# Optimization experiments

Hardware: AMD Instinct MI355X
Metric: run time of the kernel (lower is better)

## Reference

```python
import jax, jax.numpy as jnp
import numpy as np

B = 524288          # batch size
C = 64              # continuous dims
D = 8               # categorical dims
NCAT = 6            # categories per dim -> 6**8 = 1679616 total
NB = 21             # ceil(log2(6**8)) binary dims


def setup_inputs() -> dict:
    key = jax.random.key(0)
    k1, k2, k3 = jax.random.split(key, 3)
    inputs_continuous = jax.random.normal(k1, (B, C), dtype=jnp.float32)
    inputs_categorical = jax.random.randint(k2, (B, D), 0, NCAT, dtype=jnp.int32)
    # uniform dequantization noise in (0,1); keep away from 0 so log() is finite
    dequantization_noise = jax.random.uniform(k3, (B, 2 * NB), dtype=jnp.float32,
                                              minval=0.01, maxval=1.0)
    num_per_dim = jnp.full((D,), NCAT, dtype=jnp.int32)
    # category_factors[i] = prod(num_per_dim[:i]) (mixed-radix factors)
    category_factors = jnp.concatenate(
        [jnp.ones((1,), jnp.int32), jnp.cumprod(num_per_dim[:-1])]).astype(jnp.int32)
    binary_mask = (2 ** jnp.arange(NB - 1, -1, -1)).astype(jnp.int32)
    return {
        "inputs_continuous": inputs_continuous,
        "inputs_categorical": inputs_categorical,
        "dequantization_noise": dequantization_noise,
        "category_factors": category_factors,
        "binary_mask": binary_mask,
    }


def reference(inputs_continuous, inputs_categorical, dequantization_noise,
              category_factors, binary_mask):
    b = inputs_categorical.shape[0]
    nb = binary_mask.shape[0]
    # mixed-radix encode categories to a single decimal code: [B]
    decimal_encoded = jnp.sum(category_factors * inputs_categorical, axis=-1)
    # binary encode: [B, nb] bool
    binary_encoded = (decimal_encoded[:, None] & binary_mask) != 0
    # View noise as [B, nb, 2]; torch code gathers/scatters flat indices
    # 2i + (0 if bit else 1) for max slot, 2i + (1 if bit else 0) for min slot.
    view = dequantization_noise.reshape(b, nb, 2)
    v0, v1 = view[..., 0], view[..., 1]
    max_v = jnp.where(binary_encoded, v0, v1)
    min_v = jnp.where(binary_encoded, v1, v0)
    rescaling_log_probs = -jnp.sum(jnp.log(max_v), axis=-1)  # [B]
    new_min = min_v * max_v  # scatter-multiply into the min slots
    n0 = jnp.where(binary_encoded, max_v, new_min)
    n1 = jnp.where(binary_encoded, new_min, max_v)
    noise_out = jnp.stack([n0, n1], axis=-1).reshape(b, 2 * nb)
    out_continuous = jnp.concatenate([inputs_continuous, noise_out], axis=1)
    # uniform dequantizer: log prob of U(0,1) samples is 0
    dequantization_log_probs = jnp.zeros((b,), out_continuous.dtype)
    return out_continuous, dequantization_log_probs - rescaling_log_probs
```

## Files before the change

kernel.cpp:

```cpp
#include <hip/hip_runtime.h>


typedef float f4 __attribute__((ext_vector_type(4)));

constexpr int OUT_COLS = 106;
constexpr int OCTS_PER_WAVE = 2;
constexpr int WAVES = 4;
constexpr int ROWS_PER_BLOCK = WAVES * OCTS_PER_WAVE * 8;
constexpr int OUT_STAGE = 848;
constexpr int LG_STRIDE = 24;
constexpr int SLOT = OUT_STAGE + 8 * LG_STRIDE;

__global__ __launch_bounds__(256) void dequant_oct_kernel(
    const float* __restrict__ cont,
    const int*   __restrict__ cat,
    const float* __restrict__ noise,
    float* __restrict__ out,
    int B)
{
    __shared__ __align__(16) float sbuf[WAVES * OCTS_PER_WAVE * SLOT];

    const int tid  = threadIdx.x;
    const int wave = tid >> 6;
    const int lane = tid & 63;
    const int base = blockIdx.x * ROWS_PER_BLOCK + wave * (OCTS_PER_WAVE * 8);

#pragma unroll
    for (int qq = 0; qq < OCTS_PER_WAVE; ++qq) {
        const int r0 = base + 8 * qq;
        if (r0 < B) {
            float* buf = sbuf + (wave * OCTS_PER_WAVE + qq) * SLOT;
            float* lgb = buf + OUT_STAGE;

            const float* cp = cont + (size_t)r0 * 64;
            const f4 c0 = __builtin_nontemporal_load(
                reinterpret_cast<const f4*>(cp) + lane);
            const f4 c1 = __builtin_nontemporal_load(
                reinterpret_cast<const f4*>(cp) + 64 + lane);

            const float* np = noise + (size_t)r0 * 42;
            f4 n0 = __builtin_nontemporal_load(
                reinterpret_cast<const f4*>(np) + lane);
            f4 n1 = {1.f, 1.f, 1.f, 1.f};
            if (lane < 20)
                n1 = __builtin_nontemporal_load(
                    reinterpret_cast<const f4*>(np) + 64 + lane);

            int dec = 0;
            if (lane < 8) {
                const int4 a = *reinterpret_cast<const int4*>(cat + (size_t)(r0 + lane) * 8);
                const int4 b = *reinterpret_cast<const int4*>(cat + (size_t)(r0 + lane) * 8 + 4);
                dec = ((((((b.w * 6 + b.z) * 6 + b.y) * 6 + b.x) * 6
                         + a.w) * 6 + a.z) * 6 + a.y) * 6 + a.x;
            }

            auto do_pair = [&](int p, float va, float vb) {
                const int r = (p * 781) >> 14;
                const int j = p - 21 * r;
                const int dr  = __shfl(dec, r);
                const int bit = (dr >> (20 - j)) & 1;
                const float mx = bit ? va : vb;
                const float mn = bit ? vb : va;
                const float nm = mn * mx;
                float2 o;
                o.x = bit ? mx : nm;
                o.y = bit ? nm : mx;
                *reinterpret_cast<float2*>(buf + r * OUT_COLS + 64 + 2 * j) = o;
                lgb[r * LG_STRIDE + j] = __logf(mx);
            };
            do_pair(2 * lane,     n0.x, n0.y);
            do_pair(2 * lane + 1, n0.z, n0.w);
            if (lane < 20) {
                do_pair(128 + 2 * lane, n1.x, n1.y);
                do_pair(129 + 2 * lane, n1.z, n1.w);
            }

            {
                const int rr = lane >> 4;
                const int cc = 4 * (lane & 15);
                float* d0 = buf + rr * OUT_COLS + cc;
                *reinterpret_cast<float2*>(d0)     = make_float2(c0.x, c0.y);
                *reinterpret_cast<float2*>(d0 + 2) = make_float2(c0.z, c0.w);
                float* d1 = buf + (rr + 4) * OUT_COLS + cc;
                *reinterpret_cast<float2*>(d1)     = make_float2(c1.x, c1.y);
                *reinterpret_cast<float2*>(d1 + 2) = make_float2(c1.z, c1.w);
            }

            if (lane < 8) {
                const f4* lp = reinterpret_cast<const f4*>(lgb + LG_STRIDE * lane);
                const f4 a0 = lp[0], a1 = lp[1], a2 = lp[2], a3 = lp[3], a4 = lp[4];
                const float s =
                    ((a0.x + a0.y) + (a0.z + a0.w)) + ((a1.x + a1.y) + (a1.z + a1.w)) +
                    ((a2.x + a2.y) + (a2.z + a2.w)) + ((a3.x + a3.y) + (a3.z + a3.w)) +
                    ((a4.x + a4.y) + (a4.z + a4.w)) + lgb[LG_STRIDE * lane + 20];
                out[(size_t)B * OUT_COLS + r0 + lane] = s;
            }

            float* op = out + (size_t)r0 * OUT_COLS;
#pragma unroll
            for (int s4 = 0; s4 < 3; ++s4) {
                const f4 v = *reinterpret_cast<const f4*>(buf + s4 * 256 + 4 * lane);
                __builtin_nontemporal_store(
                    v, reinterpret_cast<f4*>(op + s4 * 256) + lane);
            }
            if (lane < 20) {
                const f4 v = *reinterpret_cast<const f4*>(buf + 768 + 4 * lane);
                __builtin_nontemporal_store(
                    v, reinterpret_cast<f4*>(op + 768) + lane);
            }
        }
    }
}

extern "C" void kernel_launch(void* const* d_in, const int* in_sizes, int n_in,
                              void* d_out, int out_size, void* d_ws, size_t ws_size,
                              hipStream_t stream) {
    const float* cont  = (const float*)d_in[0];
    const int*   cat   = (const int*)d_in[1];
    const float* noise = (const float*)d_in[2];

    float* out = (float*)d_out;
    const int B = in_sizes[1] / 8;

    const int grid = (B + ROWS_PER_BLOCK - 1) / ROWS_PER_BLOCK;
    dequant_oct_kernel<<<grid, 256, 0, stream>>>(cont, cat, noise, out, B);
}
```

Baseline: 79.49 us.

## Hoist both octets' loads upfront and vectorize log-prob stores via LDS

Issues all global loads for both 8-row octets before any processing, so that the second octet's memory latency overlaps with the first octet's compute. Log-prob sums are staged in LDS and written as 16-byte vector stores by four lanes instead of scalar stores from eight lanes per octet. This raises register pressure from holding two octets' data at once. The final vector store assumes both octets are valid whenever the first is, which holds only when B is a multiple of 16.

```diff
diff --git a/kernel.cpp b/kernel.cpp
--- a/kernel.cpp
+++ b/kernel.cpp
@@ -4,12 +4,13 @@
 typedef float f4 __attribute__((ext_vector_type(4)));
 
 constexpr int OUT_COLS = 106;
-constexpr int OCTS_PER_WAVE = 2;
 constexpr int WAVES = 4;
-constexpr int ROWS_PER_BLOCK = WAVES * OCTS_PER_WAVE * 8;
+constexpr int ROWS_PER_BLOCK = WAVES * 16;
 constexpr int OUT_STAGE = 848;
 constexpr int LG_STRIDE = 24;
 constexpr int SLOT = OUT_STAGE + 8 * LG_STRIDE;
+constexpr int LP_OFF = WAVES * 2 * SLOT;
+constexpr int LDS_FLOATS = LP_OFF + WAVES * 16;
 
 __global__ __launch_bounds__(256) void dequant_oct_kernel(
     const float* __restrict__ cont,
@@ -18,97 +19,115 @@
     float* __restrict__ out,
     int B)
 {
-    __shared__ __align__(16) float sbuf[WAVES * OCTS_PER_WAVE * SLOT];
+    __shared__ __align__(16) float sbuf[LDS_FLOATS];
 
     const int tid  = threadIdx.x;
     const int wave = tid >> 6;
     const int lane = tid & 63;
-    const int base = blockIdx.x * ROWS_PER_BLOCK + wave * (OCTS_PER_WAVE * 8);
+    const int r0a  = blockIdx.x * ROWS_PER_BLOCK + wave * 16;
+    const int r0b  = r0a + 8;
+    const bool okA = r0a < B, okB = r0b < B;
 
+    f4 c0a = {0,0,0,0}, c1a = {0,0,0,0}, n0a = {1,1,1,1}, n1a = {1,1,1,1};
+    f4 c0b = {0,0,0,0}, c1b = {0,0,0,0}, n0b = {1,1,1,1}, n1b = {1,1,1,1};
+    int deca = 0, decb = 0;
+
+    if (okA) {
+        const f4* cp = reinterpret_cast<const f4*>(cont + (size_t)r0a * 64);
+        c0a = __builtin_nontemporal_load(cp + lane);
+        c1a = __builtin_nontemporal_load(cp + 64 + lane);
+        const f4* np = reinterpret_cast<const f4*>(noise + (size_t)r0a * 42);
+        n0a = __builtin_nontemporal_load(np + lane);
+        if (lane < 20) n1a = __builtin_nontemporal_load(np + 64 + lane);
+        if (lane < 8) {
+            const int4 a = *reinterpret_cast<const int4*>(cat + (size_t)(r0a + lane) * 8);
+            const int4 b = *reinterpret_cast<const int4*>(cat + (size_t)(r0a + lane) * 8 + 4);
+            deca = ((((((b.w * 6 + b.z) * 6 + b.y) * 6 + b.x) * 6
+                      + a.w) * 6 + a.z) * 6 + a.y) * 6 + a.x;
+        }
+    }
+    if (okB) {
+        const f4* cp = reinterpret_cast<const f4*>(cont + (size_t)r0b * 64);
+        c0b = __builtin_nontemporal_load(cp + lane);
+        c1b = __builtin_nontemporal_load(cp + 64 + lane);
+        const f4* np = reinterpret_cast<const f4*>(noise + (size_t)r0b * 42);
+        n0b = __builtin_nontemporal_load(np + lane);
+        if (lane < 20) n1b = __builtin_nontemporal_load(np + 64 + lane);
+        if (lane < 8) {
+            const int4 a = *reinterpret_cast<const int4*>(cat + (size_t)(r0b + lane) * 8);
+            const int4 b = *reinterpret_cast<const int4*>(cat + (size_t)(r0b + lane) * 8 + 4);
+            decb = ((((((b.w * 6 + b.z) * 6 + b.y) * 6 + b.x) * 6
+                      + a.w) * 6 + a.z) * 6 + a.y) * 6 + a.x;
+        }
+    }
+
+    auto process = [&](int r0, bool ok, int slot, int dec,
+                       const f4& c0, const f4& c1, const f4& n0, const f4& n1) {
+        if (!ok) return;
+        float* buf = sbuf + slot * SLOT;
+        float* lgb = buf + OUT_STAGE;
+
+        auto do_pair = [&](int p, float va, float vb) {
+            const int r = (p * 781) >> 14;
+            const int j = p - 21 * r;
+            const int dr  = __shfl(dec, r);
+            const int bit = (dr >> (20 - j)) & 1;
+            const float mx = bit ? va : vb;
+            const float mn = bit ? vb : va;
+            const float nm = mn * mx;
+            float2 o;
+            o.x = bit ? mx : nm;
+            o.y = bit ? nm : mx;
+            *reinterpret_cast<float2*>(buf + r * OUT_COLS + 64 + 2 * j) = o;
+            lgb[r * LG_STRIDE + j] = __logf(mx);
+        };
+        do_pair(2 * lane,     n0.x, n0.y);
+        do_pair(2 * lane + 1, n0.z, n0.w);
+        if (lane < 20) {
+            do_pair(128 + 2 * lane, n1.x, n1.y);
+            do_pair(129 + 2 * lane, n1.z, n1.w);
+        }
+
+        {
+            const int rr = lane >> 4;
+            const int cc = 4 * (lane & 15);
+            float* d0 = buf + rr * OUT_COLS + cc;
+            *reinterpret_cast<float2*>(d0)     = make_float2(c0.x, c0.y);
+            *reinterpret_cast<float2*>(d0 + 2) = make_float2(c0.z, c0.w);
+            float* d1 = buf + (rr + 4) * OUT_COLS + cc;
+            *reinterpret_cast<float2*>(d1)     = make_float2(c1.x, c1.y);
+            *reinterpret_cast<float2*>(d1 + 2) = make_float2(c1.z, c1.w);
+        }
+
+        if (lane < 8) {
+            const f4* lp = reinterpret_cast<const f4*>(lgb + LG_STRIDE * lane);
+            const f4 a0 = lp[0], a1 = lp[1], a2 = lp[2], a3 = lp[3], a4 = lp[4];
+            const float s =
+                ((a0.x + a0.y) + (a0.z + a0.w)) + ((a1.x + a1.y) + (a1.z + a1.w)) +
+                ((a2.x + a2.y) + (a2.z + a2.w)) + ((a3.x + a3.y) + (a3.z + a3.w)) +
+                ((a4.x + a4.y) + (a4.z + a4.w)) + lgb[LG_STRIDE * lane + 20];
+            sbuf[LP_OFF + wave * 16 + (slot & 1) * 8 + lane] = s;
+        }
+
+        float* op = out + (size_t)r0 * OUT_COLS;
 #pragma unroll
-    for (int qq = 0; qq < OCTS_PER_WAVE; ++qq) {
-        const int r0 = base + 8 * qq;
-        if (r0 < B) {
-            float* buf = sbuf + (wave * OCTS_PER_WAVE + qq) * SLOT;
-            float* lgb = buf + OUT_STAGE;
+        for (int s4 = 0; s4 < 3; ++s4) {
+            const f4 v = *reinterpret_cast<const f4*>(buf + s4 * 256 + 4 * lane);
+            __builtin_nontemporal_store(v, reinterpret_cast<f4*>(op + s4 * 256) + lane);
+        }
+        if (lane < 20) {
+            const f4 v = *reinterpret_cast<const f4*>(buf + 768 + 4 * lane);
+            __builtin_nontemporal_store(v, reinterpret_cast<f4*>(op + 768) + lane);
+        }
+    };
 
-            const float* cp = cont + (size_t)r0 * 64;
-            const f4 c0 = __builtin_nontemporal_load(
-                reinterpret_cast<const f4*>(cp) + lane);
-            const f4 c1 = __builtin_nontemporal_load(
-                reinterpret_cast<const f4*>(cp) + 64 + lane);
+    process(r0a, okA, wave * 2,     deca, c0a, c1a, n0a, n1a);
+    process(r0b, okB, wave * 2 + 1, decb, c0b, c1b, n0b, n1b);
 
-            const float* np = noise + (size_t)r0 * 42;
-            f4 n0 = __builtin_nontemporal_load(
-                reinterpret_cast<const f4*>(np) + lane);
-            f4 n1 = {1.f, 1.f, 1.f, 1.f};
-            if (lane < 20)
-                n1 = __builtin_nontemporal_load(
-                    reinterpret_cast<const f4*>(np) + 64 + lane);
-
-            int dec = 0;
-            if (lane < 8) {
-                const int4 a = *reinterpret_cast<const int4*>(cat + (size_t)(r0 + lane) * 8);
-                const int4 b = *reinterpret_cast<const int4*>(cat + (size_t)(r0 + lane) * 8 + 4);
-                dec = ((((((b.w * 6 + b.z) * 6 + b.y) * 6 + b.x) * 6
-                         + a.w) * 6 + a.z) * 6 + a.y) * 6 + a.x;
-            }
-
-            auto do_pair = [&](int p, float va, float vb) {
-                const int r = (p * 781) >> 14;
-                const int j = p - 21 * r;
-                const int dr  = __shfl(dec, r);
-                const int bit = (dr >> (20 - j)) & 1;
-                const float mx = bit ? va : vb;
-                const float mn = bit ? vb : va;
-                const float nm = mn * mx;
-                float2 o;
-                o.x = bit ? mx : nm;
-                o.y = bit ? nm : mx;
-                *reinterpret_cast<float2*>(buf + r * OUT_COLS + 64 + 2 * j) = o;
-                lgb[r * LG_STRIDE + j] = __logf(mx);
-            };
-            do_pair(2 * lane,     n0.x, n0.y);
-            do_pair(2 * lane + 1, n0.z, n0.w);
-            if (lane < 20) {
-                do_pair(128 + 2 * lane, n1.x, n1.y);
-                do_pair(129 + 2 * lane, n1.z, n1.w);
-            }
-
-            {
-                const int rr = lane >> 4;
-                const int cc = 4 * (lane & 15);
-                float* d0 = buf + rr * OUT_COLS + cc;
-                *reinterpret_cast<float2*>(d0)     = make_float2(c0.x, c0.y);
-                *reinterpret_cast<float2*>(d0 + 2) = make_float2(c0.z, c0.w);
-                float* d1 = buf + (rr + 4) * OUT_COLS + cc;
-                *reinterpret_cast<float2*>(d1)     = make_float2(c1.x, c1.y);
-                *reinterpret_cast<float2*>(d1 + 2) = make_float2(c1.z, c1.w);
-            }
-
-            if (lane < 8) {
-                const f4* lp = reinterpret_cast<const f4*>(lgb + LG_STRIDE * lane);
-                const f4 a0 = lp[0], a1 = lp[1], a2 = lp[2], a3 = lp[3], a4 = lp[4];
-                const float s =
-                    ((a0.x + a0.y) + (a0.z + a0.w)) + ((a1.x + a1.y) + (a1.z + a1.w)) +
-                    ((a2.x + a2.y) + (a2.z + a2.w)) + ((a3.x + a3.y) + (a3.z + a3.w)) +
-                    ((a4.x + a4.y) + (a4.z + a4.w)) + lgb[LG_STRIDE * lane + 20];
-                out[(size_t)B * OUT_COLS + r0 + lane] = s;
-            }
-
-            float* op = out + (size_t)r0 * OUT_COLS;
-#pragma unroll
-            for (int s4 = 0; s4 < 3; ++s4) {
-                const f4 v = *reinterpret_cast<const f4*>(buf + s4 * 256 + 4 * lane);
-                __builtin_nontemporal_store(
-                    v, reinterpret_cast<f4*>(op + s4 * 256) + lane);
-            }
-            if (lane < 20) {
-                const f4 v = *reinterpret_cast<const f4*>(buf + 768 + 4 * lane);
-                __builtin_nontemporal_store(
-                    v, reinterpret_cast<f4*>(op + 768) + lane);
-            }
-        }
+    if (okA && lane < 4) {
+        const f4 v = *reinterpret_cast<const f4*>(sbuf + LP_OFF + wave * 16 + 4 * lane);
+        __builtin_nontemporal_store(
+            v, reinterpret_cast<f4*>(out + (size_t)B * OUT_COLS + r0a) + lane);
     }
 }
 
```

Measured after the change: 78.86 us. About the same (-0.8%).
